# Performance work log

Hardware: AMD Instinct MI355X
Metric: run time of the kernel (lower is better)

The kernel has to match this reference:

```python
import jax, jax.numpy as jnp
import numpy as np

B, D_IN, D_OUT, W = 16, 1024, 1024, 2048


def setup_inputs() -> dict:
    key = jax.random.key(0)
    kq, kk, kv, kwq, kwk, kwv = jax.random.split(key, 6)
    scale = 1.0 / np.sqrt(D_IN).astype(np.float32)
    return {
        "Q": jax.random.normal(kq, (B, D_IN, W), jnp.float32),
        "K": jax.random.normal(kk, (B, D_IN, W), jnp.float32),
        "V": jax.random.normal(kv, (B, D_IN, W), jnp.float32),
        "WQ": jax.random.normal(kwq, (D_OUT, D_IN), jnp.float32) * scale,
        "WK": jax.random.normal(kwk, (D_OUT, D_IN), jnp.float32) * scale,
        "WV": jax.random.normal(kwv, (D_OUT, D_IN), jnp.float32) * scale,
    }


def reference(Q, K, V, WQ, WK, WV):
    # Projections: M @ x with x laid out (B, d_in, seq) -> (B, d_out, seq)
    Qd = jnp.einsum('oi,bis->bos', WQ, Q)
    Kd = jnp.einsum('oi,bis->bos', WK, K)
    Vd = jnp.einsum('oi,bis->bos', WV, V)
    d_out = Qd.shape[1]
    seq = Qd.shape[2]
    # corr_mat[b, s(query), t(key)] = Q_d^T @ K_d / sqrt(d_out)
    scores = jnp.einsum('bos,bot->bst', Qd, Kd) / jnp.asarray(d_out, jnp.float32) ** 0.5
    # causal_factor = tril(-inf, diag=-1): -inf where query s > key t
    idx = jnp.arange(seq)
    mask = jnp.where(idx[:, None] > idx[None, :], -jnp.inf, 0.0).astype(scores.dtype)
    scores = scores + mask
    # NOTE: original softmaxes over dim 1 = the QUERY axis
    p = jax.nn.softmax(scores, axis=1)
    # V_d @ softmaxed -> (B, d_out, seq) indexed by key positions
    return jnp.einsum('bos,bst->bot', Vd, p)
```

## Files before the change

kernel.cpp:

```cpp
#include <hip/hip_runtime.h>
#include <cstdio>
#include <math.h>

typedef unsigned short u16;
typedef float f32x4 __attribute__((ext_vector_type(4)));
typedef __bf16 bf16x8 __attribute__((ext_vector_type(8)));
typedef u16 u16x4 __attribute__((ext_vector_type(4)));
typedef u16 u16x8 __attribute__((ext_vector_type(8)));

__device__ __forceinline__ u16 f2bf(float x) {
  unsigned u = __float_as_uint(x);
  u = (u + 0x7FFFu + ((u >> 16) & 1u)) >> 16;
  return (u16)u;
}
__device__ __forceinline__ float bf2f(u16 x) {
  return __uint_as_float(((unsigned)x) << 16);
}

__device__ __forceinline__ f32x4 mfma_bf16(bf16x8 a, bf16x8 b, f32x4 c) {
  return __builtin_amdgcn_mfma_f32_16x16x32_bf16(a, b, c, 0, 0, 0);
}

__device__ __forceinline__ void gload_lds16(const void* g, void* l) {
  __builtin_amdgcn_global_load_lds(
      (const __attribute__((address_space(1))) void*)g,
      (__attribute__((address_space(3))) void*)l, 16, 0, 0);
}

template <bool BF16OUT, bool SWZ, bool TRI, bool KLIMIT, bool SWAPXY>
__global__ __launch_bounds__(512, 2) void gemm_bt(
    const u16* __restrict__ A, const u16* __restrict__ B, void* __restrict__ Cv,
    int K, int lda, int ldb, int ldc,
    long long sAz, long long sBz, long long sCz, float scale)
{
  int bx, by, z;
  {
    const int gx = gridDim.x, gy = gridDim.y;
    const int nwg = gx * gy * gridDim.z;
    int f = blockIdx.x + gx * (blockIdx.y + gy * blockIdx.z);
    if (SWZ && (nwg & 7) == 0) f = (f & 7) * (nwg >> 3) + (f >> 3);
    if (TRI) {
      const int j = f % gx;
      z = f / gx;
      int r = (int)((sqrtf(8.f * j + 1.f) - 1.f) * 0.5f);
      while (r * (r + 1) / 2 > j) --r;
      while ((r + 1) * (r + 2) / 2 <= j) ++r;
      by = r;
      bx = j - r * (r + 1) / 2;
    } else {
      const int x = f % gx;
      const int rest = f / gx;
      const int y = rest % gy;
      z = rest / gy;
      if (SWAPXY) { bx = y; by = x; } else { bx = x; by = y; }
    }
  }

  const int n0 = bx * 256;
  const int m0 = by * 256;
  A += (long long)z * sAz;
  B += (long long)z * sBz;

  const int tid = threadIdx.x;
  const int wave = tid >> 6, lane = tid & 63;
  const int wr = wave >> 2, wc = wave & 3;

  __shared__ u16 lds[2][32768];

  f32x4 acc[8][4] = {};

  int kEnd = K;
  if (KLIMIT) { int ke = n0 + 256; kEnd = ke < K ? ke : K; }
  const int nt = kEnd >> 6;

  const int sOff = ((lane & 7) ^ ((lane >> 3) & 7)) * 8;
  const int r0 = wave * 8 + (lane >> 3);
  const u16* gA0 = A + (long long)(m0 + r0) * lda + sOff;

  const int frow = lane & 15, g = lane >> 4, swz = frow & 7;

#define AOFF(m, kk) ((wr * 128 + (m) * 16 + frow) * 64 + ((((kk) * 4 + g)) ^ swz) * 8)
#define BOFF(n, kk) (16384 + ((n) >> 1) * 8192 + (wc * 32 + ((n) & 1) * 16 + frow) * 64 + (((kk) * 4 + g) ^ swz) * 8)

#define STAGE_A(T, BUF, H)                                                     \
  {                                                                            \
    const long long kc = (long long)(T) * 64;                                  \
    _Pragma("unroll")                                                          \
    for (int c = (H) * 2; c < (H) * 2 + 2; ++c)                                \
      gload_lds16(gA0 + (long long)(c * 64) * lda + kc,                        \
                  &lds[BUF][c * 4096 + wave * 512]);                           \
  }
#define STAGE_B(T, BUF, H)                                                     \
  {                                                                            \
    const long long kc = (long long)(T) * 64;                                  \
    _Pragma("unroll")                                                          \
    for (int c = (H) * 2; c < (H) * 2 + 2; ++c) {                              \
      const int rp = (c & 1) * 64 + r0;                                        \
      const int row = (rp >> 5) * 64 + (c >> 1) * 32 + (rp & 31);              \
      gload_lds16(B + (long long)(n0 + row) * ldb + sOff + kc,                 \
                  &lds[BUF][16384 + c * 4096 + wave * 512]);                   \
    }                                                                          \
  }

  bf16x8 pA[8], pB[4];
#define READ_A(mb)                                                             \
  _Pragma("unroll")                                                            \
  for (int i = 0; i < 4; ++i) {                                                \
    pA[i * 2 + 0] = *(const bf16x8*)(bb + AOFF((mb) + i, 0));                  \
    pA[i * 2 + 1] = *(const bf16x8*)(bb + AOFF((mb) + i, 1));                  \
  }
#define READ_B(nb)                                                             \
  _Pragma("unroll")                                                            \
  for (int i = 0; i < 2; ++i) {                                                \
    pB[i * 2 + 0] = *(const bf16x8*)(bb + BOFF((nb) + i, 0));                  \
    pB[i * 2 + 1] = *(const bf16x8*)(bb + BOFF((nb) + i, 1));                  \
  }
#define MFMA16(mb, nb)                                                         \
  _Pragma("unroll")                                                            \
  for (int i = 0; i < 4; ++i)                                                  \
    _Pragma("unroll")                                                          \
    for (int j = 0; j < 2; ++j) {                                              \
      acc[(mb) + i][(nb) + j] =                                                \
          mfma_bf16(pA[i * 2 + 0], pB[j * 2 + 0], acc[(mb) + i][(nb) + j]);    \
      acc[(mb) + i][(nb) + j] =                                                \
          mfma_bf16(pA[i * 2 + 1], pB[j * 2 + 1], acc[(mb) + i][(nb) + j]);    \
    }

#define BAR()  __builtin_amdgcn_s_barrier()
#define LGKM0()                                                                \
  asm volatile("s_waitcnt lgkmcnt(0)" ::: "memory");                           \
  __builtin_amdgcn_sched_barrier(0)
#define VM(N) asm volatile("s_waitcnt vmcnt(" #N ")" ::: "memory")

  STAGE_A(0, 0, 0) STAGE_A(0, 0, 1) STAGE_B(0, 0, 0) STAGE_B(0, 0, 1)
  VM(2);
  BAR();

  for (int t = 0; t < nt; ++t) {
    const u16* bb = &lds[t & 1][0];
    const int nxb = (t + 1) & 1;
    const bool pf = (t + 1 < nt);

    READ_A(0) READ_B(0)
    if (pf) STAGE_A(t + 1, nxb, 0)
    BAR(); LGKM0();
    __builtin_amdgcn_s_setprio(1); MFMA16(0, 0); __builtin_amdgcn_s_setprio(0);
    if (pf) VM(2); else VM(0);
    BAR();

    READ_B(2)
    if (pf) STAGE_A(t + 1, nxb, 1)
    BAR(); LGKM0();
    __builtin_amdgcn_s_setprio(1); MFMA16(0, 2); __builtin_amdgcn_s_setprio(0);
    BAR();

    READ_A(4)
    if (pf) STAGE_B(t + 1, nxb, 0)
    BAR(); LGKM0();
    __builtin_amdgcn_s_setprio(1); MFMA16(4, 2); __builtin_amdgcn_s_setprio(0);
    BAR();

    READ_B(0)
    if (pf) STAGE_B(t + 1, nxb, 1)
    BAR(); LGKM0();
    __builtin_amdgcn_s_setprio(1); MFMA16(4, 0); __builtin_amdgcn_s_setprio(0);
    if (pf) VM(2); else VM(0);
    BAR();
  }
#undef STAGE_A
#undef STAGE_B
#undef READ_A
#undef READ_B
#undef MFMA16
#undef AOFF
#undef BOFF
#undef BAR
#undef LGKM0
#undef VM

  const int crow0 = m0 + wr * 128 + (lane >> 4) * 4;
  const int ccol0 = n0 + wc * 64 + (lane & 15);
  if (BF16OUT) {
    u16* C = (u16*)Cv + (long long)z * sCz;
#pragma unroll
    for (int m = 0; m < 8; ++m)
#pragma unroll
      for (int n = 0; n < 4; ++n)
#pragma unroll
        for (int r = 0; r < 4; ++r)
          C[(long long)(crow0 + m * 16 + r) * ldc + ccol0 + n * 16] = f2bf(acc[m][n][r] * scale);
  } else {
    float* C = (float*)Cv + (long long)z * sCz;
#pragma unroll
    for (int m = 0; m < 8; ++m)
#pragma unroll
      for (int n = 0; n < 4; ++n)
#pragma unroll
        for (int r = 0; r < 4; ++r)
          C[(long long)(crow0 + m * 16 + r) * ldc + ccol0 + n * 16] = acc[m][n][r] * scale;
  }
}

__global__ __launch_bounds__(256) void conv_transpose(const float* __restrict__ src, u16* __restrict__ dst)
{
  const int b = blockIdx.z;
  const float* s = src + (long long)b * 1024 * 2048;
  u16* d = dst + (long long)b * 2048 * 1024;
  const int s0 = blockIdx.x * 64, i0 = blockIdx.y * 64;
  const int tx = threadIdx.x, ty = threadIdx.y;
  __shared__ float tile[64][65];
#pragma unroll
  for (int r = 0; r < 16; ++r)
    tile[r * 4 + ty][tx] = s[(long long)(i0 + r * 4 + ty) * 2048 + s0 + tx];
  __syncthreads();
#pragma unroll
  for (int r = 0; r < 16; ++r)
    d[(long long)(s0 + r * 4 + ty) * 1024 + i0 + tx] = f2bf(tile[tx][r * 4 + ty]);
}

__global__ __launch_bounds__(256) void conv_weights(
    const float* __restrict__ a, const float* __restrict__ b, const float* __restrict__ c,
    u16* __restrict__ oa, u16* __restrict__ ob, u16* __restrict__ oc)
{
  const int which = blockIdx.y;
  const float* s = which == 0 ? a : which == 1 ? b : c;
  u16* d = which == 0 ? oa : which == 1 ? ob : oc;
  const int idx = (blockIdx.x * 256 + threadIdx.x) * 4;
  f32x4 v = *(const f32x4*)(s + idx);
  u16x4 o;
#pragma unroll
  for (int j = 0; j < 4; ++j) o[j] = f2bf(v[j]);
  *(u16x4*)(d + idx) = o;
}

__global__ __launch_bounds__(256) void col_softmax(const u16* __restrict__ S, u16* __restrict__ P)
{
  const int t = blockIdx.x;
  const long long rowOff = ((long long)blockIdx.y * 2048 + t) * 2048;
  const u16* row = S + rowOff;
  u16* prow = P + rowOff;
  const int tid = threadIdx.x;
  const int i0 = tid * 8;

  u16x8 a = *(const u16x8*)(row + i0);
  float v[8];
#pragma unroll
  for (int j = 0; j < 8; ++j)
    v[j] = (i0 + j <= t) ? bf2f(a[j]) : -1e30f;

  float m = v[0];
#pragma unroll
  for (int j = 1; j < 8; ++j) m = fmaxf(m, v[j]);
#pragma unroll
  for (int off = 32; off; off >>= 1) m = fmaxf(m, __shfl_xor(m, off));
  __shared__ float red[4];
  __shared__ float red2[4];
  if ((tid & 63) == 0) red[tid >> 6] = m;
  __syncthreads();
  m = fmaxf(fmaxf(red[0], red[1]), fmaxf(red[2], red[3]));

  float e[8]; float ssum = 0.f;
#pragma unroll
  for (int j = 0; j < 8; ++j) { e[j] = __expf(v[j] - m); ssum += e[j]; }
#pragma unroll
  for (int off = 32; off; off >>= 1) ssum += __shfl_xor(ssum, off);
  if ((tid & 63) == 0) red2[tid >> 6] = ssum;
  __syncthreads();
  ssum = red2[0] + red2[1] + red2[2] + red2[3];
  const float inv = 1.0f / ssum;
  u16x8 o;
#pragma unroll
  for (int j = 0; j < 8; ++j) o[j] = f2bf(e[j] * inv);
  *(u16x8*)(prow + i0) = o;
}

extern "C" void kernel_launch(void* const* d_in, const int* in_sizes, int n_in,
                              void* d_out, int out_size, void* d_ws, size_t ws_size,
                              hipStream_t stream)
{
  const float* Q  = (const float*)d_in[0];
  const float* K  = (const float*)d_in[1];
  const float* V  = (const float*)d_in[2];
  const float* WQ = (const float*)d_in[3];
  const float* WK = (const float*)d_in[4];
  const float* WV = (const float*)d_in[5];
  float* out = (float*)d_out;

  const size_t MB = 1ull << 20;
  char* w = (char*)d_ws;
  if (ws_size < 262 * MB) {
    fprintf(stderr, "kernel_launch: workspace too small (%zu B, need >= %zu B)\n",
            ws_size, (size_t)(262 * MB));
    return;
  }

  u16* wq    = (u16*)(w + 0 * MB);
  u16* wk    = (u16*)(w + 2 * MB);
  u16* wv    = (u16*)(w + 4 * MB);
  u16* qdt   = (u16*)(w + 6 * MB);
  u16* kdt   = (u16*)(w + 70 * MB);
  u16* vd    = (u16*)(w + 134 * MB);
  u16* trans = (u16*)(w + 198 * MB);
  u16* S     = (u16*)(w + 198 * MB);

  long long freeMB = (long long)(ws_size / MB) - 198;
  int chunk = (int)(freeMB / 16);
  if (chunk > 8) chunk = 8;
  u16* P = (u16*)(w + (198 + (size_t)chunk * 8) * MB);

  conv_weights<<<dim3(1024, 3), 256, 0, stream>>>(WQ, WK, WV, wq, wk, wv);

  conv_transpose<<<dim3(32, 16, 16), dim3(64, 4), 0, stream>>>(Q, trans);
  gemm_bt<true, true, false, false, false><<<dim3(4, 128, 1), 512, 0, stream>>>(
      trans, wq, qdt, 1024, 1024, 1024, 1024, 0, 0, 0, 1.0f);
  conv_transpose<<<dim3(32, 16, 16), dim3(64, 4), 0, stream>>>(K, trans);
  gemm_bt<true, true, false, false, false><<<dim3(4, 128, 1), 512, 0, stream>>>(
      trans, wk, kdt, 1024, 1024, 1024, 1024, 0, 0, 0, 1.0f);
  conv_transpose<<<dim3(32, 16, 16), dim3(64, 4), 0, stream>>>(V, trans);
  gemm_bt<true, true, false, false, false><<<dim3(8, 4, 16), 512, 0, stream>>>(
      wv, trans, vd, 1024, 1024, 1024, 2048,
      0, (long long)2048 * 1024, (long long)1024 * 2048, 1.0f);

  for (int b0 = 0; b0 < 16; b0 += chunk) {
    const int nb = (16 - b0) < chunk ? (16 - b0) : chunk;
    gemm_bt<true, true, true, false, false><<<dim3(36, 1, nb), 512, 0, stream>>>(
        kdt + (long long)b0 * 2048 * 1024, qdt + (long long)b0 * 2048 * 1024, S,
        1024, 1024, 1024, 2048,
        (long long)2048 * 1024, (long long)2048 * 1024, (long long)2048 * 2048, 0.03125f);
    col_softmax<<<dim3(2048, nb), 256, 0, stream>>>(S, P);
    gemm_bt<false, true, false, true, true><<<dim3(4, 8, nb), 512, 0, stream>>>(
        vd + (long long)b0 * 1024 * 2048, P, out + (long long)b0 * 1024 * 2048,
        2048, 2048, 2048, 2048,
        (long long)1024 * 2048, (long long)2048 * 2048, (long long)1024 * 2048, 1.0f);
  }
}
```

Measured before the change: 640.5 us.

## Process all batches at once and split PV GEMM along causal K

Removes the per-chunk batch loop so the score GEMM, column softmax and PV GEMM each launch once over all 16 batches, with softmax writing in place into the score buffer. The PV GEMM is split into two launches covering halves of the causal K range, ordered longest tiles first, with the second launch accumulating into the output. This aims to cut launch count and improve load balance of the triangular PV work. In exchange it needs a larger workspace, adds an extra read-modify-write pass over the fp32 output, and relies on in-place softmax being safe.

Measured after the change: 669.3 us. +4.5%, slower.

```diff
diff --git a/kernel.cpp b/kernel.cpp
--- a/kernel.cpp
+++ b/kernel.cpp
@@ -27,14 +27,21 @@
       (__attribute__((address_space(3))) void*)l, 16, 0, 0);
 }
 
-template <bool BF16OUT, bool SWZ, bool TRI, bool KLIMIT, bool SWAPXY>
+template <bool BF16OUT, bool SWZ, bool TRI, int PVK>
 __global__ __launch_bounds__(512, 2) void gemm_bt(
     const u16* __restrict__ A, const u16* __restrict__ B, void* __restrict__ Cv,
     int K, int lda, int ldb, int ldc,
     long long sAz, long long sBz, long long sCz, float scale)
 {
-  int bx, by, z;
-  {
+  int bx, by, z, kt0, ktN;
+  if (PVK >= 0) {
+    const int tb = 7 - (int)blockIdx.z;
+    bx = tb; by = (int)blockIdx.y; z = (int)blockIdx.x;
+    const int ntFull = (tb + 1) * 4;
+    const int nA = (ntFull + 1) >> 1;
+    kt0 = (PVK == 0) ? 0 : nA;
+    ktN = (PVK == 0) ? nA : ntFull;
+  } else {
     const int gx = gridDim.x, gy = gridDim.y;
     const int nwg = gx * gy * gridDim.z;
     int f = blockIdx.x + gx * (blockIdx.y + gy * blockIdx.z);
@@ -48,12 +55,12 @@
       by = r;
       bx = j - r * (r + 1) / 2;
     } else {
-      const int x = f % gx;
+      bx = f % gx;
       const int rest = f / gx;
-      const int y = rest % gy;
+      by = rest % gy;
       z = rest / gy;
-      if (SWAPXY) { bx = y; by = x; } else { bx = x; by = y; }
     }
+    kt0 = 0; ktN = K >> 6;
   }
 
   const int n0 = bx * 256;
@@ -69,9 +76,7 @@
 
   f32x4 acc[8][4] = {};
 
-  int kEnd = K;
-  if (KLIMIT) { int ke = n0 + 256; kEnd = ke < K ? ke : K; }
-  const int nt = kEnd >> 6;
+  const int nt = ktN - kt0;
 
   const int sOff = ((lane & 7) ^ ((lane >> 3) & 7)) * 8;
   const int r0 = wave * 8 + (lane >> 3);
@@ -132,36 +137,37 @@
   __builtin_amdgcn_sched_barrier(0)
 #define VM(N) asm volatile("s_waitcnt vmcnt(" #N ")" ::: "memory")
 
-  STAGE_A(0, 0, 0) STAGE_A(0, 0, 1) STAGE_B(0, 0, 0) STAGE_B(0, 0, 1)
+  STAGE_A(kt0, 0, 0) STAGE_A(kt0, 0, 1) STAGE_B(kt0, 0, 0) STAGE_B(kt0, 0, 1)
   VM(2);
   BAR();
 
-  for (int t = 0; t < nt; ++t) {
-    const u16* bb = &lds[t & 1][0];
-    const int nxb = (t + 1) & 1;
-    const bool pf = (t + 1 < nt);
+  for (int i2 = 0; i2 < nt; ++i2) {
+    const u16* bb = &lds[i2 & 1][0];
+    const int nxb = (i2 + 1) & 1;
+    const bool pf = (i2 + 1 < nt);
+    const int tn = kt0 + i2 + 1;
 
     READ_A(0) READ_B(0)
-    if (pf) STAGE_A(t + 1, nxb, 0)
+    if (pf) STAGE_A(tn, nxb, 0)
     BAR(); LGKM0();
     __builtin_amdgcn_s_setprio(1); MFMA16(0, 0); __builtin_amdgcn_s_setprio(0);
     if (pf) VM(2); else VM(0);
     BAR();
 
     READ_B(2)
-    if (pf) STAGE_A(t + 1, nxb, 1)
+    if (pf) STAGE_A(tn, nxb, 1)
     BAR(); LGKM0();
     __builtin_amdgcn_s_setprio(1); MFMA16(0, 2); __builtin_amdgcn_s_setprio(0);
     BAR();
 
     READ_A(4)
-    if (pf) STAGE_B(t + 1, nxb, 0)
+    if (pf) STAGE_B(tn, nxb, 0)
     BAR(); LGKM0();
     __builtin_amdgcn_s_setprio(1); MFMA16(4, 2); __builtin_amdgcn_s_setprio(0);
     BAR();
 
     READ_B(0)
-    if (pf) STAGE_B(t + 1, nxb, 1)
+    if (pf) STAGE_B(tn, nxb, 1)
     BAR(); LGKM0();
     __builtin_amdgcn_s_setprio(1); MFMA16(4, 0); __builtin_amdgcn_s_setprio(0);
     if (pf) VM(2); else VM(0);
@@ -191,13 +197,25 @@
           C[(long long)(crow0 + m * 16 + r) * ldc + ccol0 + n * 16] = f2bf(acc[m][n][r] * scale);
   } else {
     float* C = (float*)Cv + (long long)z * sCz;
-#pragma unroll
-    for (int m = 0; m < 8; ++m)
-#pragma unroll
-      for (int n = 0; n < 4; ++n)
-#pragma unroll
-        for (int r = 0; r < 4; ++r)
-          C[(long long)(crow0 + m * 16 + r) * ldc + ccol0 + n * 16] = acc[m][n][r] * scale;
+    if (PVK == 1) {
+#pragma unroll
+      for (int m = 0; m < 8; ++m)
+#pragma unroll
+        for (int n = 0; n < 4; ++n)
+#pragma unroll
+          for (int r = 0; r < 4; ++r) {
+            const long long off = (long long)(crow0 + m * 16 + r) * ldc + ccol0 + n * 16;
+            C[off] += acc[m][n][r] * scale;
+          }
+    } else {
+#pragma unroll
+      for (int m = 0; m < 8; ++m)
+#pragma unroll
+        for (int n = 0; n < 4; ++n)
+#pragma unroll
+          for (int r = 0; r < 4; ++r)
+            C[(long long)(crow0 + m * 16 + r) * ldc + ccol0 + n * 16] = acc[m][n][r] * scale;
+    }
   }
 }
 
@@ -288,9 +306,9 @@
 
   const size_t MB = 1ull << 20;
   char* w = (char*)d_ws;
-  if (ws_size < 262 * MB) {
+  if (ws_size < 326 * MB) {
     fprintf(stderr, "kernel_launch: workspace too small (%zu B, need >= %zu B)\n",
-            ws_size, (size_t)(262 * MB));
+            ws_size, (size_t)(326 * MB));
     return;
   }
 
@@ -303,34 +321,27 @@
   u16* trans = (u16*)(w + 198 * MB);
   u16* S     = (u16*)(w + 198 * MB);
 
-  long long freeMB = (long long)(ws_size / MB) - 198;
-  int chunk = (int)(freeMB / 16);
-  if (chunk > 8) chunk = 8;
-  u16* P = (u16*)(w + (198 + (size_t)chunk * 8) * MB);
-
   conv_weights<<<dim3(1024, 3), 256, 0, stream>>>(WQ, WK, WV, wq, wk, wv);
 
   conv_transpose<<<dim3(32, 16, 16), dim3(64, 4), 0, stream>>>(Q, trans);
-  gemm_bt<true, true, false, false, false><<<dim3(4, 128, 1), 512, 0, stream>>>(
+  gemm_bt<true, true, false, -1><<<dim3(4, 128, 1), 512, 0, stream>>>(
       trans, wq, qdt, 1024, 1024, 1024, 1024, 0, 0, 0, 1.0f);
   conv_transpose<<<dim3(32, 16, 16), dim3(64, 4), 0, stream>>>(K, trans);
-  gemm_bt<true, true, false, false, false><<<dim3(4, 128, 1), 512, 0, stream>>>(
+  gemm_bt<true, true, false, -1><<<dim3(4, 128, 1), 512, 0, stream>>>(
       trans, wk, kdt, 1024, 1024, 1024, 1024, 0, 0, 0, 1.0f);
   conv_transpose<<<dim3(32, 16, 16), dim3(64, 4), 0, stream>>>(V, trans);
-  gemm_bt<true, true, false, false, false><<<dim3(8, 4, 16), 512, 0, stream>>>(
+  gemm_bt<true, true, false, -1><<<dim3(8, 4, 16), 512, 0, stream>>>(
       wv, trans, vd, 1024, 1024, 1024, 2048,
       0, (long long)2048 * 1024, (long long)1024 * 2048, 1.0f);
 
-  for (int b0 = 0; b0 < 16; b0 += chunk) {
-    const int nb = (16 - b0) < chunk ? (16 - b0) : chunk;
-    gemm_bt<true, true, true, false, false><<<dim3(36, 1, nb), 512, 0, stream>>>(
-        kdt + (long long)b0 * 2048 * 1024, qdt + (long long)b0 * 2048 * 1024, S,
-        1024, 1024, 1024, 2048,
-        (long long)2048 * 1024, (long long)2048 * 1024, (long long)2048 * 2048, 0.03125f);
-    col_softmax<<<dim3(2048, nb), 256, 0, stream>>>(S, P);
-    gemm_bt<false, true, false, true, true><<<dim3(4, 8, nb), 512, 0, stream>>>(
-        vd + (long long)b0 * 1024 * 2048, P, out + (long long)b0 * 1024 * 2048,
-        2048, 2048, 2048, 2048,
-        (long long)1024 * 2048, (long long)2048 * 2048, (long long)1024 * 2048, 1.0f);
-  }
-}
+  gemm_bt<true, true, true, -1><<<dim3(36, 1, 16), 512, 0, stream>>>(
+      kdt, qdt, S, 1024, 1024, 1024, 2048,
+      (long long)2048 * 1024, (long long)2048 * 1024, (long long)2048 * 2048, 0.03125f);
+  col_softmax<<<dim3(2048, 16), 256, 0, stream>>>(S, S);
+  gemm_bt<false, false, false, 0><<<dim3(16, 4, 8), 512, 0, stream>>>(
+      vd, S, out, 2048, 2048, 2048, 2048,
+      (long long)1024 * 2048, (long long)2048 * 2048, (long long)1024 * 2048, 1.0f);
+  gemm_bt<false, false, false, 1><<<dim3(16, 4, 8), 512, 0, stream>>>(
+      vd, S, out, 2048, 2048, 2048, 2048,
+      (long long)1024 * 2048, (long long)2048 * 2048, (long long)1024 * 2048, 1.0f);
+}
```

## Fuse fp32 transpose-convert into projection GEMMs and drop batch chunking

Applied to the files above, without the earlier changes.

Removes the separate conv_transpose kernels. The projection GEMMs now load fp32 activations directly, convert them to bf16 in registers and write them transposed into swizzled LDS, which avoids a round trip through global memory for the transposed copies. All 16 batches are processed in single launches, with the softmax done in place on S. The PV GEMM uses a new grid mapping that dispatches the longest-K tiles first. In exchange, the register-staged path waits on vmcnt(0) each iteration, so it overlaps loads and compute less than the async global-to-LDS path did, and the kernel now needs a larger workspace.

After: 566.4 us. -11.6%, faster.

```diff
diff --git a/kernel.cpp b/kernel.cpp
--- a/kernel.cpp
+++ b/kernel.cpp
@@ -27,14 +27,17 @@
       (__attribute__((address_space(3))) void*)l, 16, 0, 0);
 }
 
-template <bool BF16OUT, bool SWZ, bool TRI, bool KLIMIT, bool SWAPXY>
+template <bool BF16OUT, bool SWZ, bool TRI, bool KLIMIT, bool PVLPT, int TMODE>
 __global__ __launch_bounds__(512, 2) void gemm_bt(
-    const u16* __restrict__ A, const u16* __restrict__ B, void* __restrict__ Cv,
+    const u16* __restrict__ A, const u16* __restrict__ B,
+    const float* __restrict__ Tf, void* __restrict__ Cv,
     int K, int lda, int ldb, int ldc,
     long long sAz, long long sBz, long long sCz, float scale)
 {
   int bx, by, z;
-  {
+  if (PVLPT) {
+    z = (int)blockIdx.x; by = (int)blockIdx.y; bx = 7 - (int)blockIdx.z;
+  } else {
     const int gx = gridDim.x, gy = gridDim.y;
     const int nwg = gx * gy * gridDim.z;
     int f = blockIdx.x + gx * (blockIdx.y + gy * blockIdx.z);
@@ -48,11 +51,10 @@
       by = r;
       bx = j - r * (r + 1) / 2;
     } else {
-      const int x = f % gx;
+      bx = f % gx;
       const int rest = f / gx;
-      const int y = rest % gy;
+      by = rest % gy;
       z = rest / gy;
-      if (SWAPXY) { bx = y; by = x; } else { bx = x; by = y; }
     }
   }
 
@@ -70,17 +72,29 @@
   f32x4 acc[8][4] = {};
 
   int kEnd = K;
-  if (KLIMIT) { int ke = n0 + 256; kEnd = ke < K ? ke : K; }
+  if (KLIMIT || PVLPT) { int ke = n0 + 256; kEnd = ke < K ? ke : K; }
   const int nt = kEnd >> 6;
 
   const int sOff = ((lane & 7) ^ ((lane >> 3) & 7)) * 8;
   const int r0 = wave * 8 + (lane >> 3);
   const u16* gA0 = A + (long long)(m0 + r0) * lda + sOff;
 
-  const int frow = lane & 15, g = lane >> 4, swz = frow & 7;
-
-#define AOFF(m, kk) ((wr * 128 + (m) * 16 + frow) * 64 + ((((kk) * 4 + g)) ^ swz) * 8)
-#define BOFF(n, kk) (16384 + ((n) >> 1) * 8192 + (wc * 32 + ((n) & 1) * 16 + frow) * 64 + (((kk) * 4 + g) ^ swz) * 8)
+  const float* Tsrc = nullptr;
+  if (TMODE == 1) Tsrc = Tf + ((long long)(m0 >> 11) * 1024) * 2048 + (m0 & 2047);
+  else if (TMODE == 2) Tsrc = Tf + ((long long)z * 1024) * 2048 + n0;
+  const int tcol = lane * 4;
+  f32x4 tv[8];
+
+  const int frow = lane & 15, g = lane >> 4;
+  const int swzA0 = (TMODE == 1) ? ((frow & 7) ^ (frow >> 2)) : (frow & 7);
+  const int swzA1 = (TMODE == 1) ? ((frow & 7) ^ (4 + (frow >> 2))) : (frow & 7);
+  const int swzB0 = (TMODE == 2) ? ((frow & 7) ^ (frow >> 2)) : (frow & 7);
+  const int swzB1 = (TMODE == 2) ? ((frow & 7) ^ (4 + (frow >> 2))) : (frow & 7);
+
+#define AOFF(m, kk) ((wr * 128 + (m) * 16 + frow) * 64 + \
+                     (((kk) * 4 + g) ^ (((m) & 1) ? swzA1 : swzA0)) * 8)
+#define BOFF(n, kk) (16384 + ((n) >> 1) * 8192 + (wc * 32 + ((n) & 1) * 16 + frow) * 64 + \
+                     (((kk) * 4 + g) ^ (((n) & 1) ? swzB1 : swzB0)) * 8)
 
 #define STAGE_A(T, BUF, H)                                                     \
   {                                                                            \
@@ -101,6 +115,27 @@
                   &lds[BUF][16384 + c * 4096 + wave * 512]);                   \
     }                                                                          \
   }
+#define TLOAD(T)                                                               \
+  _Pragma("unroll")                                                            \
+  for (int r = 0; r < 8; ++r)                                                  \
+    tv[r] = *(const f32x4*)(Tsrc + (long long)((T) * 64 + wave * 8 + r) * 2048 + tcol);
+#define TCVT(BUF)                                                              \
+  _Pragma("unroll")                                                            \
+  for (int j = 0; j < 4; ++j) {                                                \
+    const int rw = (lane << 2) + j;                                            \
+    u16x8 hv;                                                                  \
+    _Pragma("unroll")                                                          \
+    for (int r = 0; r < 8; ++r) hv[r] = f2bf(tv[r][j]);                        \
+    int ad;                                                                    \
+    if (TMODE == 1) {                                                          \
+      ad = rw * 64 + ((wave ^ ((rw & 7) ^ ((rw >> 2) & 7))) * 8);              \
+    } else {                                                                   \
+      const int h = (rw >> 5) & 1, rp = (rw >> 6) * 32 + (rw & 31);            \
+      ad = 16384 + h * 8192 + rp * 64 +                                        \
+           ((wave ^ ((rp & 7) ^ ((rp >> 2) & 7))) * 8);                        \
+    }                                                                          \
+    *(u16x8*)(&lds[BUF][ad]) = hv;                                             \
+  }
 
   bf16x8 pA[8], pB[4];
 #define READ_A(mb)                                                             \
@@ -132,43 +167,92 @@
   __builtin_amdgcn_sched_barrier(0)
 #define VM(N) asm volatile("s_waitcnt vmcnt(" #N ")" ::: "memory")
 
-  STAGE_A(0, 0, 0) STAGE_A(0, 0, 1) STAGE_B(0, 0, 0) STAGE_B(0, 0, 1)
-  VM(2);
-  BAR();
-
-  for (int t = 0; t < nt; ++t) {
-    const u16* bb = &lds[t & 1][0];
-    const int nxb = (t + 1) & 1;
-    const bool pf = (t + 1 < nt);
-
-    READ_A(0) READ_B(0)
-    if (pf) STAGE_A(t + 1, nxb, 0)
-    BAR(); LGKM0();
-    __builtin_amdgcn_s_setprio(1); MFMA16(0, 0); __builtin_amdgcn_s_setprio(0);
-    if (pf) VM(2); else VM(0);
+  if constexpr (TMODE == 0) {
+    STAGE_A(0, 0, 0) STAGE_A(0, 0, 1) STAGE_B(0, 0, 0) STAGE_B(0, 0, 1)
+    VM(2);
     BAR();
-
-    READ_B(2)
-    if (pf) STAGE_A(t + 1, nxb, 1)
-    BAR(); LGKM0();
-    __builtin_amdgcn_s_setprio(1); MFMA16(0, 2); __builtin_amdgcn_s_setprio(0);
+    for (int t = 0; t < nt; ++t) {
+      const u16* bb = &lds[t & 1][0];
+      const int nxb = (t + 1) & 1;
+      const bool pf = (t + 1 < nt);
+
+      READ_A(0) READ_B(0)
+      if (pf) STAGE_A(t + 1, nxb, 0)
+      BAR(); LGKM0();
+      __builtin_amdgcn_s_setprio(1); MFMA16(0, 0); __builtin_amdgcn_s_setprio(0);
+      if (pf) VM(2); else VM(0);
+      BAR();
+
+      READ_B(2)
+      if (pf) STAGE_A(t + 1, nxb, 1)
+      BAR(); LGKM0();
+      __builtin_amdgcn_s_setprio(1); MFMA16(0, 2); __builtin_amdgcn_s_setprio(0);
+      BAR();
+
+      READ_A(4)
+      if (pf) STAGE_B(t + 1, nxb, 0)
+      BAR(); LGKM0();
+      __builtin_amdgcn_s_setprio(1); MFMA16(4, 2); __builtin_amdgcn_s_setprio(0);
+      BAR();
+
+      READ_B(0)
+      if (pf) STAGE_B(t + 1, nxb, 1)
+      BAR(); LGKM0();
+      __builtin_amdgcn_s_setprio(1); MFMA16(4, 0); __builtin_amdgcn_s_setprio(0);
+      if (pf) VM(2); else VM(0);
+      BAR();
+    }
+  } else {
+    TLOAD(0)
+    if (TMODE == 1) { STAGE_B(0, 0, 0) STAGE_B(0, 0, 1) }
+    else            { STAGE_A(0, 0, 0) STAGE_A(0, 0, 1) }
+    VM(0);
+    TCVT(0)
+    asm volatile("s_waitcnt lgkmcnt(0)" ::: "memory");
     BAR();
-
-    READ_A(4)
-    if (pf) STAGE_B(t + 1, nxb, 0)
-    BAR(); LGKM0();
-    __builtin_amdgcn_s_setprio(1); MFMA16(4, 2); __builtin_amdgcn_s_setprio(0);
-    BAR();
-
-    READ_B(0)
-    if (pf) STAGE_B(t + 1, nxb, 1)
-    BAR(); LGKM0();
-    __builtin_amdgcn_s_setprio(1); MFMA16(4, 0); __builtin_amdgcn_s_setprio(0);
-    if (pf) VM(2); else VM(0);
-    BAR();
+    for (int t = 0; t < nt; ++t) {
+      const u16* bb = &lds[t & 1][0];
+      const int nxb = (t + 1) & 1;
+      const bool pf = (t + 1 < nt);
+
+      if (pf) {
+        TLOAD(t + 1)
+        if (TMODE == 1) { STAGE_B(t + 1, nxb, 0) STAGE_B(t + 1, nxb, 1) }
+        else            { STAGE_A(t + 1, nxb, 0) STAGE_A(t + 1, nxb, 1) }
+      }
+
+      READ_A(0) READ_B(0)
+      BAR(); LGKM0();
+      __builtin_amdgcn_s_setprio(1); MFMA16(0, 0); __builtin_amdgcn_s_setprio(0);
+      BAR();
+
+      READ_B(2)
+      BAR(); LGKM0();
+      __builtin_amdgcn_s_setprio(1); MFMA16(0, 2); __builtin_amdgcn_s_setprio(0);
+      BAR();
+
+      READ_A(4)
+      BAR(); LGKM0();
+      __builtin_amdgcn_s_setprio(1); MFMA16(4, 2); __builtin_amdgcn_s_setprio(0);
+      BAR();
+
+      READ_B(0)
+      BAR(); LGKM0();
+      __builtin_amdgcn_s_setprio(1); MFMA16(4, 0); __builtin_amdgcn_s_setprio(0);
+      if (pf) {
+        VM(0);
+        TCVT(nxb)
+      } else {
+        VM(0);
+      }
+      asm volatile("s_waitcnt lgkmcnt(0)" ::: "memory");
+      BAR();
+    }
   }
 #undef STAGE_A
 #undef STAGE_B
+#undef TLOAD
+#undef TCVT
 #undef READ_A
 #undef READ_B
 #undef MFMA16
@@ -199,23 +283,6 @@
         for (int r = 0; r < 4; ++r)
           C[(long long)(crow0 + m * 16 + r) * ldc + ccol0 + n * 16] = acc[m][n][r] * scale;
   }
-}
-
-__global__ __launch_bounds__(256) void conv_transpose(const float* __restrict__ src, u16* __restrict__ dst)
-{
-  const int b = blockIdx.z;
-  const float* s = src + (long long)b * 1024 * 2048;
-  u16* d = dst + (long long)b * 2048 * 1024;
-  const int s0 = blockIdx.x * 64, i0 = blockIdx.y * 64;
-  const int tx = threadIdx.x, ty = threadIdx.y;
-  __shared__ float tile[64][65];
-#pragma unroll
-  for (int r = 0; r < 16; ++r)
-    tile[r * 4 + ty][tx] = s[(long long)(i0 + r * 4 + ty) * 2048 + s0 + tx];
-  __syncthreads();
-#pragma unroll
-  for (int r = 0; r < 16; ++r)
-    d[(long long)(s0 + r * 4 + ty) * 1024 + i0 + tx] = f2bf(tile[tx][r * 4 + ty]);
 }
 
 __global__ __launch_bounds__(256) void conv_weights(
@@ -288,49 +355,35 @@
 
   const size_t MB = 1ull << 20;
   char* w = (char*)d_ws;
-  if (ws_size < 262 * MB) {
+  if (ws_size < 326 * MB) {
     fprintf(stderr, "kernel_launch: workspace too small (%zu B, need >= %zu B)\n",
-            ws_size, (size_t)(262 * MB));
+            ws_size, (size_t)(326 * MB));
     return;
   }
 
-  u16* wq    = (u16*)(w + 0 * MB);
-  u16* wk    = (u16*)(w + 2 * MB);
-  u16* wv    = (u16*)(w + 4 * MB);
-  u16* qdt   = (u16*)(w + 6 * MB);
-  u16* kdt   = (u16*)(w + 70 * MB);
-  u16* vd    = (u16*)(w + 134 * MB);
-  u16* trans = (u16*)(w + 198 * MB);
-  u16* S     = (u16*)(w + 198 * MB);
-
-  long long freeMB = (long long)(ws_size / MB) - 198;
-  int chunk = (int)(freeMB / 16);
-  if (chunk > 8) chunk = 8;
-  u16* P = (u16*)(w + (198 + (size_t)chunk * 8) * MB);
+  u16* wq  = (u16*)(w + 0 * MB);
+  u16* wk  = (u16*)(w + 2 * MB);
+  u16* wv  = (u16*)(w + 4 * MB);
+  u16* qdt = (u16*)(w + 6 * MB);
+  u16* kdt = (u16*)(w + 70 * MB);
+  u16* vd  = (u16*)(w + 134 * MB);
+  u16* S   = (u16*)(w + 198 * MB);
 
   conv_weights<<<dim3(1024, 3), 256, 0, stream>>>(WQ, WK, WV, wq, wk, wv);
 
-  conv_transpose<<<dim3(32, 16, 16), dim3(64, 4), 0, stream>>>(Q, trans);
-  gemm_bt<true, true, false, false, false><<<dim3(4, 128, 1), 512, 0, stream>>>(
-      trans, wq, qdt, 1024, 1024, 1024, 1024, 0, 0, 0, 1.0f);
-  conv_transpose<<<dim3(32, 16, 16), dim3(64, 4), 0, stream>>>(K, trans);
-  gemm_bt<true, true, false, false, false><<<dim3(4, 128, 1), 512, 0, stream>>>(
-      trans, wk, kdt, 1024, 1024, 1024, 1024, 0, 0, 0, 1.0f);
-  conv_transpose<<<dim3(32, 16, 16), dim3(64, 4), 0, stream>>>(V, trans);
-  gemm_bt<true, true, false, false, false><<<dim3(8, 4, 16), 512, 0, stream>>>(
-      wv, trans, vd, 1024, 1024, 1024, 2048,
-      0, (long long)2048 * 1024, (long long)1024 * 2048, 1.0f);
-
-  for (int b0 = 0; b0 < 16; b0 += chunk) {
-    const int nb = (16 - b0) < chunk ? (16 - b0) : chunk;
-    gemm_bt<true, true, true, false, false><<<dim3(36, 1, nb), 512, 0, stream>>>(
-        kdt + (long long)b0 * 2048 * 1024, qdt + (long long)b0 * 2048 * 1024, S,
-        1024, 1024, 1024, 2048,
-        (long long)2048 * 1024, (long long)2048 * 1024, (long long)2048 * 2048, 0.03125f);
-    col_softmax<<<dim3(2048, nb), 256, 0, stream>>>(S, P);
-    gemm_bt<false, true, false, true, true><<<dim3(4, 8, nb), 512, 0, stream>>>(
-        vd + (long long)b0 * 1024 * 2048, P, out + (long long)b0 * 1024 * 2048,
-        2048, 2048, 2048, 2048,
-        (long long)1024 * 2048, (long long)2048 * 2048, (long long)1024 * 2048, 1.0f);
-  }
-}
+  gemm_bt<true, true, false, false, false, 1><<<dim3(4, 128, 1), 512, 0, stream>>>(
+      wq, wq, Q, qdt, 1024, 0, 1024, 1024, 0, 0, 0, 1.0f);
+  gemm_bt<true, true, false, false, false, 1><<<dim3(4, 128, 1), 512, 0, stream>>>(
+      wk, wk, K, kdt, 1024, 0, 1024, 1024, 0, 0, 0, 1.0f);
+  gemm_bt<true, true, false, false, false, 2><<<dim3(8, 4, 16), 512, 0, stream>>>(
+      wv, wv, V, vd, 1024, 1024, 0, 2048,
+      0, 0, (long long)1024 * 2048, 1.0f);
+
+  gemm_bt<true, true, true, false, false, 0><<<dim3(36, 1, 16), 512, 0, stream>>>(
+      kdt, qdt, nullptr, S, 1024, 1024, 1024, 2048,
+      (long long)2048 * 1024, (long long)2048 * 1024, (long long)2048 * 2048, 0.03125f);
+  col_softmax<<<dim3(2048, 16), 256, 0, stream>>>(S, S);
+  gemm_bt<false, false, false, true, true, 0><<<dim3(16, 4, 8), 512, 0, stream>>>(
+      vd, S, nullptr, out, 2048, 2048, 2048, 2048,
+      (long long)1024 * 2048, (long long)2048 * 2048, (long long)1024 * 2048, 1.0f);
+}
```
